# Kernel optimization log

Hardware: AMD Instinct MI355X
Metric: run time of the kernel (lower is better)

## Reference

```python
import jax, jax.numpy as jnp
import numpy as np

IN_DIM = 256
HID = 384
HEADS = 6
NH1 = HID // HEADS  # 64 per-head hidden in layer1
N = 3072
SLOPE_GAT = 0.2   # LeakyReLU inside GAT attention
SLOPE_ACT = 0.01  # default nn.LeakyReLU / F.leaky_relu slope


def _leaky(x, s):
    return jnp.where(x >= 0, x, s * x)


def _gat_sublayer(h, mask, W, a, heads, nh, concat):
    # h: [N, F_in], mask: [N, N] bool, W: [heads*nh, F_in], a: [2*nh]
    n = h.shape[0]
    g = (h @ W.T).reshape(n, heads, nh)  # [N, H, F]
    # e[i,j,h] = leakyrelu(<g_i, a_l> + <g_j, a_r>)  (avoids O(N^2) concat)
    sl = jnp.einsum('nhf,f->nh', g, a[:nh])
    sr = jnp.einsum('nhf,f->nh', g, a[nh:])
    e = _leaky(sl[:, None, :] + sr[None, :, :], SLOPE_GAT)  # [N, N, H]
    e = jnp.where(mask[:, :, None], e, jnp.float32(-10000.0))
    att = jax.nn.softmax(e, axis=1)  # softmax over source nodes j
    out = jnp.einsum('ijh,jhf->ihf', att, g)
    return out.reshape(n, heads * nh) if concat else out.mean(axis=1)


def _gat(x, mask, W1, a1, W2, a2):
    x = _gat_sublayer(x, mask, W1, a1, HEADS, NH1, True)   # [N, HID]
    x = jax.nn.elu(x)
    return _gat_sublayer(x, mask, W2, a2, 1, IN_DIM, False)  # [N, IN_DIM]


def setup_inputs() -> dict:
    key = jax.random.key(0)
    ks = iter(jax.random.split(key, 32))
    d = {
        'feature': jax.random.normal(next(ks), (1, N, IN_DIM), jnp.float32),
        'adj': jax.random.randint(next(ks), (1, N, N), 0, 2, jnp.int32),
        'doc_num': 16,
        'sect_num': 192,
    }
    def w(shape, scale=0.05):
        return jax.random.normal(next(ks), shape, jnp.float32) * scale
    for br in ('sent', 'sect', 'doc'):
        d[f'W1_{br}'] = w((HID, IN_DIM))
        d[f'a1_{br}'] = w((2 * NH1,))
        d[f'W2_{br}'] = w((IN_DIM, HID))
        d[f'a2_{br}'] = w((2 * IN_DIM,))
    d['fusion_W'] = w((IN_DIM, 3 * IN_DIM)); d['fusion_b'] = jnp.zeros((IN_DIM,), jnp.float32)
    d['ffn_W0'] = w((HID, IN_DIM)); d['ffn_b0'] = jnp.zeros((HID,), jnp.float32)
    d['ffn_W1'] = w((HID, HID)); d['ffn_b1'] = jnp.zeros((HID,), jnp.float32)
    d['ffn_W2'] = w((IN_DIM, HID)); d['ffn_b2'] = jnp.zeros((IN_DIM,), jnp.float32)
    return d


def reference(feature, adj, doc_num, sect_num,
              W1_sent, a1_sent, W2_sent, a2_sent,
              W1_sect, a1_sect, W2_sect, a2_sect,
              W1_doc, a1_doc, W2_doc, a2_doc,
              fusion_W, fusion_b,
              ffn_W0, ffn_b0, ffn_W1, ffn_b1, ffn_W2, ffn_b2):
    f = feature[0]          # [N, D]
    n = f.shape[0]
    A = adj[0] != 0         # [N, N]
    cols = jnp.arange(n)
    sent_mask = A & (cols < n - sect_num - doc_num)[None, :]
    sect_mask = A & (cols >= n - sect_num - doc_num)[None, :] & (cols < n - doc_num)[None, :]
    doc_mask = A & (cols >= n - doc_num)[None, :]

    f_sent = _gat(f, sent_mask, W1_sent, a1_sent, W2_sent, a2_sent) + f
    f_sect = _gat(f, sect_mask, W1_sect, a1_sect, W2_sect, a2_sect) + f
    f_doc = _gat(f, doc_mask, W1_doc, a1_doc, W2_doc, a2_doc) + f

    fused = jnp.concatenate([f_doc, f_sect, f_sent], axis=-1)  # [N, 3D]
    fused = _leaky(fused @ fusion_W.T + fusion_b, SLOPE_ACT)
    h = _leaky(fused @ ffn_W0.T + ffn_b0, SLOPE_ACT)
    h = _leaky(h @ ffn_W1.T + ffn_b1, SLOPE_ACT)
    h = _leaky(h @ ffn_W2.T + ffn_b2, SLOPE_ACT)
    return (h + f)[None]    # [1, N, D]
```

## Files before the change

### kernel.cpp

```cpp
#include <hip/hip_runtime.h>
#include <stdint.h>

#define N_NODES 3072
#define D_IN    256
#define HIDDEN  384
#define HEADS   6
#define NH1     64
#define C1      1152
#define C2      768
#define MASK_ULL   48
#define MASK_BYTES 384
#define MASK_BSTRIDE ((size_t)N_NODES * MASK_BYTES)
#define CHUNK   1536
#define MAXQ    2
#define LOG2E   1.4426950408889634f

typedef __bf16 bf16;
typedef __bf16 bf16x8 __attribute__((ext_vector_type(8)));
typedef __bf16 bf16x4 __attribute__((ext_vector_type(4)));
typedef float  f32x4  __attribute__((ext_vector_type(4)));

__device__ __forceinline__ void atomAddF(float* p, float v) {
  __hip_atomic_fetch_add(p, v, __ATOMIC_RELAXED, __HIP_MEMORY_SCOPE_AGENT);
}
__device__ __forceinline__ float fexp2(float x) {
  float r; asm("v_exp_f32 %0, %1" : "=v"(r) : "v"(x)); return r;
}

struct CastArgs {
  const float* src[11];
  bf16*        dst[11];
  int          cum4[12];
};

__global__ __launch_bounds__(256) void cast_all_kernel(CastArgs A) {
  int g = blockIdx.x * 256 + threadIdx.x;
  int j = 0;
#pragma unroll
  for (int k = 1; k < 11; ++k) j += (g >= A.cum4[k]);
  int e = (g - A.cum4[j]) * 4;
  float4 v = *(const float4*)(A.src[j] + e);
  bf16x4 o = { (bf16)v.x, (bf16)v.y, (bf16)v.z, (bf16)v.w };
  *(bf16x4*)(A.dst[j] + e) = o;
}

__global__ __launch_bounds__(256) void pack_adj_kernel(const int* __restrict__ adj,
                                                       unsigned long long* __restrict__ maskU,
                                                       const int* __restrict__ dnum,
                                                       const int* __restrict__ snum) {
  int dn = dnum[0], sn = snum[0];
  int bb1 = N_NODES - sn - dn, bb2 = N_NODES - dn;
  int row = blockIdx.x;
  const int* ar = adj + (size_t)row * N_NODES;
  int lane = threadIdx.x & 63, wave = threadIdx.x >> 6;
#pragma unroll
  for (int it = 0; it < N_NODES / 256; ++it) {
    int j = it * 256 + wave * 64 + lane;
    bool a = ar[j] != 0;
    unsigned long long m0 = __ballot(a && (j < bb1));
    unsigned long long m1 = __ballot(a && (j >= bb1) && (j < bb2));
    unsigned long long m2 = __ballot(a && (j >= bb2));
    if (lane == 0) {
      size_t o = (size_t)row * MASK_ULL + it * 4 + wave;
      maskU[o] = m0;
      maskU[o + (size_t)N_NODES * MASK_ULL] = m1;
      maskU[o + 2 * (size_t)N_NODES * MASK_ULL] = m2;
    }
  }
}

template<int C>
__global__ __launch_bounds__(256) void pack_kernel(const bf16* __restrict__ src,
                                                   bf16* __restrict__ dst) {
  __shared__ bf16 t[64][72];
  int j0 = blockIdx.x * 64, f0 = blockIdx.y * 64;
  int rr = threadIdx.x >> 4;
  int cc = (threadIdx.x & 15) * 4;
#pragma unroll
  for (int p = 0; p < 4; ++p) {
    int r = p * 16 + rr;
    *(bf16x4*)&t[r][cc] = *(const bf16x4*)&src[(size_t)(j0 + r) * C + f0 + cc];
  }
  __syncthreads();
  int f = threadIdx.x & 63, g = threadIdx.x >> 6;
#pragma unroll
  for (int q = 0; q < 2; ++q) {
    int p = g * 2 + q;
    bf16x8 v = { t[p*8+0][f], t[p*8+1][f], t[p*8+2][f], t[p*8+3][f],
                 t[p*8+4][f], t[p*8+5][f], t[p*8+6][f], t[p*8+7][f] };
    *(bf16x8*)&dst[ ((size_t)((j0 >> 3) + p) * C + f0 + f) * 8 ] = v;
  }
}

template<int NHEADS, int NH>
__global__ __launch_bounds__(256) void head_proj_kernel(
    const bf16* __restrict__ g, int ldg,
    const float* __restrict__ a0, const float* __restrict__ a1, const float* __restrict__ a2,
    float* __restrict__ sl, float* __restrict__ sr) {
  int tid = blockIdx.x * 256 + threadIdx.x;
  int c = tid / N_NODES, i = tid - c * N_NODES;
  int b = c / NHEADS, h = c - b * NHEADS;
  const float* a = (b == 0) ? a0 : (b == 1) ? a1 : a2;
  const bf16* gr = g + (size_t)i * ldg + b * (NHEADS * NH) + h * NH;
  float accl = 0.f, accr = 0.f;
#pragma unroll 4
  for (int f = 0; f < NH; f += 4) {
    bf16x4 v = *(const bf16x4*)&gr[f];
#pragma unroll
    for (int k = 0; k < 4; ++k) {
      float gv = (float)v[k];
      accl += gv * a[f + k];
      accr += gv * a[NH + f + k];
    }
  }
  sl[c * N_NODES + i] = accl * LOG2E;
  sr[c * N_NODES + i] = accr * LOG2E;
}

__global__ __launch_bounds__(256) void colmean_kernel(const bf16* __restrict__ g, int C,
                                                      float* __restrict__ out) {
  int c = blockIdx.x * 256 + threadIdx.x;
  if (c >= C) return;
  int r0 = blockIdx.y * 128;
  float s = 0.f;
  for (int r = r0; r < r0 + 128; ++r) s += (float)g[(size_t)r * C + c];
  atomAddF(&out[c], s * (1.0f / N_NODES));
}

template<bool BIAS, bool LEAKY, bool RES, bool F32OUT>
__global__ __launch_bounds__(256) void gemm64_kernel(
    const bf16* __restrict__ A, int lda, int aZoff,
    const bf16* __restrict__ B0, const bf16* __restrict__ B1, const bf16* __restrict__ B2,
    int ldb, void* __restrict__ Cout, int ldc, int cZoff, int K,
    const float* __restrict__ bias, const float* __restrict__ res) {
  __shared__ bf16 As[64 * 64];
  __shared__ bf16 Bs[64 * 64];
  int z = blockIdx.z;
  const bf16* Ab = A + (size_t)z * aZoff;
  const bf16* Bb = (z == 0) ? B0 : (z == 1) ? B1 : B2;
  int m0 = blockIdx.x * 64, n0 = blockIdx.y * 64;
  int tid = threadIdx.x;
  int lane = tid & 63, wave = tid >> 6;
  int wm = wave >> 1, wn = wave & 1;
  int l15 = lane & 15, lk = lane >> 4;
  f32x4 acc[2][2] = {};
  for (int kt = 0; kt < K; kt += 64) {
#pragma unroll
    for (int h = 0; h < 2; ++h) {
      int u = h * 256 + tid;
      int r = u >> 3, up = u & 7;
      int ul = up ^ (r & 7);
      *(bf16x8*)&As[r * 64 + up * 8] = *(const bf16x8*)&Ab[(size_t)(m0 + r) * lda + kt + ul * 8];
      *(bf16x8*)&Bs[r * 64 + up * 8] = *(const bf16x8*)&Bb[(size_t)(n0 + r) * ldb + kt + ul * 8];
    }
    __syncthreads();
#pragma unroll
    for (int s = 0; s < 2; ++s) {
      bf16x8 af[2], bfr[2];
      int u = s * 4 + lk;
#pragma unroll
      for (int mi = 0; mi < 2; ++mi) {
        int r = wm * 32 + mi * 16 + l15;
        af[mi] = *(const bf16x8*)&As[r * 64 + (u ^ (r & 7)) * 8];
      }
#pragma unroll
      for (int ni = 0; ni < 2; ++ni) {
        int r = wn * 32 + ni * 16 + l15;
        bfr[ni] = *(const bf16x8*)&Bs[r * 64 + (u ^ (r & 7)) * 8];
      }
#pragma unroll
      for (int mi = 0; mi < 2; ++mi)
#pragma unroll
        for (int ni = 0; ni < 2; ++ni)
          acc[mi][ni] = __builtin_amdgcn_mfma_f32_16x16x32_bf16(af[mi], bfr[ni], acc[mi][ni], 0, 0, 0);
    }
    __syncthreads();
  }
#pragma unroll
  for (int mi = 0; mi < 2; ++mi)
#pragma unroll
    for (int ni = 0; ni < 2; ++ni)
#pragma unroll
      for (int r = 0; r < 4; ++r) {
        int i = m0 + wm * 32 + mi * 16 + lk * 4 + r;
        int col = z * cZoff + n0 + wn * 32 + ni * 16 + l15;
        float v = acc[mi][ni][r];
        if (BIAS) v += bias[col];
        if (LEAKY) v = (v >= 0.f) ? v : 0.01f * v;
        if (RES) v += res[(size_t)i * ldc + col];
        if (F32OUT) ((float*)Cout)[(size_t)i * ldc + col] = v;
        else        ((bf16*)Cout)[(size_t)i * ldc + col] = (bf16)v;
      }
}

template<bool L1>
__global__ __launch_bounds__(256) void att_kernel(
    const bf16* __restrict__ gP, const float* __restrict__ slA, const float* __restrict__ srA,
    const unsigned char* __restrict__ maskB,
    const int* __restrict__ dnum, const int* __restrict__ snum,
    float* __restrict__ accP, float* __restrict__ lP) {
  constexpr int C = L1 ? C1 : C2;
  int c = blockIdx.y;
  int b = L1 ? (c / 6) : (c >> 2);
  int colbase = L1 ? c * 64 : (b * 256 + (c & 3) * 64);
  int sidx = L1 ? c : b;
  int q = blockIdx.z;
  int dn = dnum[0], sn = snum[0];
  int bb1 = N_NODES - sn - dn, bb2 = N_NODES - dn;
  int jlo = (b == 0) ? 0 : (b == 1) ? bb1 : bb2;
  int jhi = (b == 0) ? bb1 : (b == 1) ? bb2 : N_NODES;
  int lo32 = jlo & ~31, hi32 = (jhi + 31) & ~31;
  int qlo = q * CHUNK, qhi = qlo + CHUNK;
  int wlo = max(lo32, qlo), whi = min(hi32, qhi);
  if (wlo >= whi) return;

  int wave = threadIdx.x >> 6, lane = threadIdx.x & 63;
  int l15 = lane & 15, lk = lane >> 4;
  int row0 = blockIdx.x * 64 + wave * 16;
  int ip = row0 + l15;
  float sl = slA[sidx * N_NODES + ip];
  const float* srp = srA + sidx * N_NODES;
  const unsigned char* mrow = maskB + (size_t)b * MASK_BSTRIDE + (size_t)ip * MASK_BYTES;
  bf16x8 ones;
#pragma unroll
  for (int e = 0; e < 8; ++e) ones[e] = (bf16)1.0f;
  f32x4 acc[4] = {};
  f32x4 accl = {};
  for (int jt = wlo; jt < whi; jt += 32) {
    int jb = jt + lk * 8;
    unsigned int mb = mrow[jb >> 3];
    float4 s0 = *(const float4*)&srp[jb];
    float4 s1 = *(const float4*)&srp[jb + 4];
    float sv[8] = { s0.x, s0.y, s0.z, s0.w, s1.x, s1.y, s1.z, s1.w };
    bf16x8 a8;
#pragma unroll
    for (int e = 0; e < 8; ++e) {
      float x = sl + sv[e];
      x = fmaf(fminf(x, 0.f), -0.8f, x);
      float p = fexp2(x);
      p = ((mb >> e) & 1u) ? p : 0.f;
      a8[e] = (bf16)p;
    }
    size_t pbase = (size_t)(jb >> 3) * C * 8;
#pragma unroll
    for (int nf = 0; nf < 4; ++nf) {
      bf16x8 b8 = *(const bf16x8*)&gP[pbase + (size_t)(colbase + nf * 16 + l15) * 8];
      acc[nf] = __builtin_amdgcn_mfma_f32_16x16x32_bf16(a8, b8, acc[nf], 0, 0, 0);
    }
    accl = __builtin_amdgcn_mfma_f32_16x16x32_bf16(a8, ones, accl, 0, 0, 0);
  }
  int slot = c * MAXQ + q;
  float* ap = accP + ((size_t)slot * N_NODES + row0) * 64;
#pragma unroll
  for (int nf = 0; nf < 4; ++nf)
#pragma unroll
    for (int r = 0; r < 4; ++r)
      ap[(lk * 4 + r) * 64 + nf * 16 + l15] = acc[nf][r];
  if (l15 == 0) {
#pragma unroll
    for (int r = 0; r < 4; ++r)
      lP[(size_t)slot * N_NODES + row0 + lk * 4 + r] = accl[r];
  }
}

__global__ __launch_bounds__(256) void fin1_kernel(
    const float* __restrict__ accP, const float* __restrict__ lP,
    const float* __restrict__ gm, const int* __restrict__ dnum, const int* __restrict__ snum,
    bf16* __restrict__ out1) {
  int t = blockIdx.x * 256 + threadIdx.x;
  int i = t / (C1 / 8), f0 = (t - i * (C1 / 8)) * 8;
  int c = f0 >> 6;
  int b = c / 6;
  int dn = dnum[0], sn = snum[0];
  int bb1 = N_NODES - sn - dn, bb2 = N_NODES - dn;
  int jlo = (b == 0) ? 0 : (b == 1) ? bb1 : bb2;
  int jhi = (b == 0) ? bb1 : (b == 1) ? bb2 : N_NODES;
  float l = 0.f;
  float a[8] = {0.f,0.f,0.f,0.f,0.f,0.f,0.f,0.f};
  if (jhi > jlo) {
    int q0 = jlo / CHUNK, q1 = (jhi - 1) / CHUNK;
    for (int q = q0; q <= q1; ++q) {
      int slot = c * MAXQ + q;
      l += lP[(size_t)slot * N_NODES + i];
      const float* ap = &accP[((size_t)slot * N_NODES + i) * 64 + (f0 & 63)];
      f32x4 v0 = *(const f32x4*)ap, v1 = *(const f32x4*)(ap + 4);
#pragma unroll
      for (int e = 0; e < 4; ++e) { a[e] += v0[e]; a[e + 4] += v1[e]; }
    }
  }
  float inv = (l > 0.f) ? 1.f / l : 0.f;
  bf16x8 o;
#pragma unroll
  for (int e = 0; e < 8; ++e) {
    float v = (l > 0.f) ? a[e] * inv : gm[f0 + e];
    v = (v > 0.f) ? v : (__expf(v) - 1.f);
    o[e] = (bf16)v;
  }
  *(bf16x8*)&out1[(size_t)i * C1 + f0] = o;
}

__global__ __launch_bounds__(256) void fin2_kernel(
    const float* __restrict__ accP, const float* __restrict__ lP,
    const float* __restrict__ gm, const float* __restrict__ feat,
    const int* __restrict__ dnum, const int* __restrict__ snum,
    bf16* __restrict__ fused) {
  int t = blockIdx.x * 256 + threadIdx.x;
  int i = t / (C2 / 8), f0 = (t - i * (C2 / 8)) * 8;
  int b = f0 >> 8;
  int fi = f0 & 255;
  int fc = (f0 >> 6) & 3;
  int c = b * 4 + fc;
  int dn = dnum[0], sn = snum[0];
  int bb1 = N_NODES - sn - dn, bb2 = N_NODES - dn;
  int jlo = (b == 0) ? 0 : (b == 1) ? bb1 : bb2;
  int jhi = (b == 0) ? bb1 : (b == 1) ? bb2 : N_NODES;
  float l = 0.f;
  float a[8] = {0.f,0.f,0.f,0.f,0.f,0.f,0.f,0.f};
  if (jhi > jlo) {
    int q0 = jlo / CHUNK, q1 = (jhi - 1) / CHUNK;
    for (int q = q0; q <= q1; ++q) {
      int slot = c * MAXQ + q;
      l += lP[(size_t)slot * N_NODES + i];
      const float* ap = &accP[((size_t)slot * N_NODES + i) * 64 + (f0 & 63)];
      f32x4 v0 = *(const f32x4*)ap, v1 = *(const f32x4*)(ap + 4);
#pragma unroll
      for (int e = 0; e < 4; ++e) { a[e] += v0[e]; a[e + 4] += v1[e]; }
    }
  }
  float inv = (l > 0.f) ? 1.f / l : 0.f;
  bf16x8 o;
#pragma unroll
  for (int e = 0; e < 8; ++e) {
    float v = (l > 0.f) ? a[e] * inv : gm[f0 + e];
    v += feat[(size_t)i * D_IN + fi + e];
    o[e] = (bf16)v;
  }
  *(bf16x8*)&fused[(size_t)i * C2 + (2 - b) * D_IN + fi] = o;
}

extern "C" void kernel_launch(void* const* d_in, const int* in_sizes, int n_in,
                              void* d_out, int out_size, void* d_ws, size_t ws_size,
                              hipStream_t stream) {
  (void)in_sizes; (void)n_in; (void)out_size; (void)ws_size;
  const float* feature = (const float*)d_in[0];
  const int*   adj     = (const int*)d_in[1];
  const int*   dnum    = (const int*)d_in[2];
  const int*   snum    = (const int*)d_in[3];
  const float* W1s = (const float*)d_in[4];  const float* a1s = (const float*)d_in[5];
  const float* W2s = (const float*)d_in[6];  const float* a2s = (const float*)d_in[7];
  const float* W1e = (const float*)d_in[8];  const float* a1e = (const float*)d_in[9];
  const float* W2e = (const float*)d_in[10]; const float* a2e = (const float*)d_in[11];
  const float* W1d = (const float*)d_in[12]; const float* a1d = (const float*)d_in[13];
  const float* W2d = (const float*)d_in[14]; const float* a2d = (const float*)d_in[15];
  const float* fW  = (const float*)d_in[16]; const float* fB  = (const float*)d_in[17];
  const float* w0  = (const float*)d_in[18]; const float* b0  = (const float*)d_in[19];
  const float* w1  = (const float*)d_in[20]; const float* b1  = (const float*)d_in[21];
  const float* w2  = (const float*)d_in[22]; const float* b2  = (const float*)d_in[23];

  char* ws = (char*)d_ws;
  size_t off = 0;
  auto alloc = [&](size_t bytes) { void* p = ws + off; off += (bytes + 255) & ~(size_t)255; return p; };

  unsigned long long* maskU = (unsigned long long*)alloc(3 * (size_t)N_NODES * MASK_ULL * 8);
  bf16* fbf   = (bf16*)alloc((size_t)N_NODES * D_IN * 2);
  bf16* w1b0  = (bf16*)alloc(HIDDEN * D_IN * 2);
  bf16* w1b1  = (bf16*)alloc(HIDDEN * D_IN * 2);
  bf16* w1b2  = (bf16*)alloc(HIDDEN * D_IN * 2);
  bf16* w2b0  = (bf16*)alloc(D_IN * HIDDEN * 2);
  bf16* w2b1  = (bf16*)alloc(D_IN * HIDDEN * 2);
  bf16* w2b2  = (bf16*)alloc(D_IN * HIDDEN * 2);
  bf16* wfusb = (bf16*)alloc(D_IN * C2 * 2);
  bf16* wf0b  = (bf16*)alloc(HIDDEN * D_IN * 2);
  bf16* wf1b  = (bf16*)alloc(HIDDEN * HIDDEN * 2);
  bf16* wf2b  = (bf16*)alloc(D_IN * HIDDEN * 2);
  bf16* g1    = (bf16*)alloc((size_t)N_NODES * C1 * 2);
  bf16* gP1   = (bf16*)alloc((size_t)N_NODES * C1 * 2);
  bf16* out1  = (bf16*)alloc((size_t)N_NODES * C1 * 2);
  bf16* g2    = (bf16*)alloc((size_t)N_NODES * C2 * 2);
  bf16* gP2   = (bf16*)alloc((size_t)N_NODES * C2 * 2);
  bf16* fusedB= (bf16*)alloc((size_t)N_NODES * C2 * 2);
  bf16* h0    = (bf16*)alloc((size_t)N_NODES * D_IN * 2);
  bf16* h1    = (bf16*)alloc((size_t)N_NODES * HIDDEN * 2);
  bf16* h2    = (bf16*)alloc((size_t)N_NODES * HIDDEN * 2);
  float* sl1  = (float*)alloc(18 * N_NODES * 4);
  float* sr1  = (float*)alloc(18 * N_NODES * 4);
  float* sl2  = (float*)alloc(3 * N_NODES * 4);
  float* sr2  = (float*)alloc(3 * N_NODES * 4);
  float* accU = (float*)alloc((size_t)18 * MAXQ * N_NODES * 64 * 4);
  float* lU   = (float*)alloc((size_t)18 * MAXQ * N_NODES * 4);
  size_t zoff = off;
  float* gm1  = (float*)alloc(C1 * 4);
  float* gm2  = (float*)alloc(C2 * 4);
  size_t zbytes = off - zoff;
  const unsigned char* maskBytes = (const unsigned char*)maskU;

  hipMemsetAsync(ws + zoff, 0, zbytes, stream);

  CastArgs ca;
  {
    const float* srcs[11] = { feature, W1s, W1e, W1d, W2s, W2e, W2d, fW, w0, w1, w2 };
    bf16* dsts[11] = { fbf, w1b0, w1b1, w1b2, w2b0, w2b1, w2b2, wfusb, wf0b, wf1b, wf2b };
    int counts[11] = { N_NODES*D_IN, HIDDEN*D_IN, HIDDEN*D_IN, HIDDEN*D_IN,
                       D_IN*HIDDEN, D_IN*HIDDEN, D_IN*HIDDEN, D_IN*C2,
                       HIDDEN*D_IN, HIDDEN*HIDDEN, D_IN*HIDDEN };
    int cum = 0;
    for (int k = 0; k < 11; ++k) { ca.src[k] = srcs[k]; ca.dst[k] = dsts[k]; ca.cum4[k] = cum; cum += counts[k] / 4; }
    ca.cum4[11] = cum;
    cast_all_kernel<<<cum / 256, 256, 0, stream>>>(ca);
  }
  pack_adj_kernel<<<N_NODES, 256, 0, stream>>>(adj, maskU, dnum, snum);
  gemm64_kernel<false,false,false,false><<<dim3(48,6,3), 256, 0, stream>>>(
      fbf, D_IN, 0, w1b0, w1b1, w1b2, D_IN, g1, C1, HIDDEN, D_IN, nullptr, nullptr);
  pack_kernel<C1><<<dim3(48,18), 256, 0, stream>>>(g1, gP1);
  head_proj_kernel<HEADS, NH1><<<18 * N_NODES / 256, 256, 0, stream>>>(g1, C1, a1s, a1e, a1d, sl1, sr1);
  colmean_kernel<<<dim3((C1 + 255) / 256, 24), 256, 0, stream>>>(g1, C1, gm1);
  att_kernel<true><<<dim3(48, 18, MAXQ), 256, 0, stream>>>(gP1, sl1, sr1, maskBytes, dnum, snum, accU, lU);
  fin1_kernel<<<N_NODES * (C1 / 8) / 256, 256, 0, stream>>>(accU, lU, gm1, dnum, snum, out1);
  gemm64_kernel<false,false,false,false><<<dim3(48,4,3), 256, 0, stream>>>(
      out1, C1, HIDDEN, w2b0, w2b1, w2b2, HIDDEN, g2, C2, D_IN, HIDDEN, nullptr, nullptr);
  pack_kernel<C2><<<dim3(48,12), 256, 0, stream>>>(g2, gP2);
  head_proj_kernel<1, D_IN><<<3 * N_NODES / 256, 256, 0, stream>>>(g2, C2, a2s, a2e, a2d, sl2, sr2);
  colmean_kernel<<<dim3((C2 + 255) / 256, 24), 256, 0, stream>>>(g2, C2, gm2);
  att_kernel<false><<<dim3(48, 12, MAXQ), 256, 0, stream>>>(gP2, sl2, sr2, maskBytes, dnum, snum, accU, lU);
  fin2_kernel<<<N_NODES * (C2 / 8) / 256, 256, 0, stream>>>(accU, lU, gm2, feature, dnum, snum, fusedB);
  gemm64_kernel<true,true,false,false><<<dim3(48,4,1), 256, 0, stream>>>(
      fusedB, C2, 0, wfusb, wfusb, wfusb, C2, h0, D_IN, 0, C2, fB, nullptr);
  gemm64_kernel<true,true,false,false><<<dim3(48,6,1), 256, 0, stream>>>(
      h0, D_IN, 0, wf0b, wf0b, wf0b, D_IN, h1, HIDDEN, 0, D_IN, b0, nullptr);
  gemm64_kernel<true,true,false,false><<<dim3(48,6,1), 256, 0, stream>>>(
      h1, HIDDEN, 0, wf1b, wf1b, wf1b, HIDDEN, h2, HIDDEN, 0, HIDDEN, b1, nullptr);
  gemm64_kernel<true,true,true,true><<<dim3(48,4,1), 256, 0, stream>>>(
      h2, HIDDEN, 0, wf2b, wf2b, wf2b, HIDDEN, d_out, D_IN, 0, HIDDEN, b2, feature);
}
```

Measured before the change: 310.9 us.

## Factor attention exponentials per node and rebalance source-range split across branches

Replaces the per-edge exp2 of the LeakyReLU score with products of precomputed per-node exponentials (exp(sl)*exp(sr) or their 0.2-scaled versions), chosen by comparing against 1. The source range is now split into four chunks only for the large sentence branch, while the short section and doc ranges get a single chunk, with new slot indexing in the finalize kernels. Head projection is parallelised with 16 lanes per row and a shuffle reduction. This removes transcendental work from the inner loop at the cost of two extra loads per element, and it risks overflow or precision loss because no max is subtracted.

```diff
diff --git a/kernel.cpp b/kernel.cpp
--- a/kernel.cpp
+++ b/kernel.cpp
@@ -11,8 +11,7 @@
 #define MASK_ULL   48
 #define MASK_BYTES 384
 #define MASK_BSTRIDE ((size_t)N_NODES * MASK_BYTES)
-#define CHUNK   1536
-#define MAXQ    2
+#define QS      4
 #define LOG2E   1.4426950408889634f
 
 typedef __bf16 bf16;
@@ -25,6 +24,9 @@
 }
 __device__ __forceinline__ float fexp2(float x) {
   float r; asm("v_exp_f32 %0, %1" : "=v"(r) : "v"(x)); return r;
+}
+__device__ __forceinline__ int bnd32(int jlo, int jhi, int len, int q, int Qb) {
+  return (q >= Qb) ? ((jhi + 31) & ~31) : ((jlo + (len * q) / Qb) & ~31);
 }
 
 struct CastArgs {
@@ -92,29 +94,41 @@
   }
 }
 
-template<int NHEADS, int NH>
+template<int NCPB, int NH>
 __global__ __launch_bounds__(256) void head_proj_kernel(
     const bf16* __restrict__ g, int ldg,
     const float* __restrict__ a0, const float* __restrict__ a1, const float* __restrict__ a2,
-    float* __restrict__ sl, float* __restrict__ sr) {
-  int tid = blockIdx.x * 256 + threadIdx.x;
-  int c = tid / N_NODES, i = tid - c * N_NODES;
-  int b = c / NHEADS, h = c - b * NHEADS;
+    float* __restrict__ elp, float* __restrict__ eln,
+    float* __restrict__ erp, float* __restrict__ ern) {
+  int c = blockIdx.y;
+  int i = blockIdx.x * 16 + (threadIdx.x >> 4);
+  int b = c / NCPB;
   const float* a = (b == 0) ? a0 : (b == 1) ? a1 : a2;
-  const bf16* gr = g + (size_t)i * ldg + b * (NHEADS * NH) + h * NH;
+  int f0 = (threadIdx.x & 15) * (NH / 16);
+  const bf16* gr = g + (size_t)i * ldg + c * NH + f0;
   float accl = 0.f, accr = 0.f;
-#pragma unroll 4
-  for (int f = 0; f < NH; f += 4) {
-    bf16x4 v = *(const bf16x4*)&gr[f];
-#pragma unroll
-    for (int k = 0; k < 4; ++k) {
-      float gv = (float)v[k];
-      accl += gv * a[f + k];
-      accr += gv * a[NH + f + k];
-    }
-  }
-  sl[c * N_NODES + i] = accl * LOG2E;
-  sr[c * N_NODES + i] = accr * LOG2E;
+#pragma unroll
+  for (int k = 0; k < NH / 16; k += 4) {
+    bf16x4 v = *(const bf16x4*)&gr[k];
+#pragma unroll
+    for (int e = 0; e < 4; ++e) {
+      float gv = (float)v[e];
+      accl += gv * a[f0 + k + e];
+      accr += gv * a[NH + f0 + k + e];
+    }
+  }
+#pragma unroll
+  for (int m = 1; m < 16; m <<= 1) {
+    accl += __shfl_xor(accl, m, 64);
+    accr += __shfl_xor(accr, m, 64);
+  }
+  if ((threadIdx.x & 15) == 0) {
+    int o = c * N_NODES + i;
+    elp[o] = fexp2(accl * LOG2E);
+    eln[o] = fexp2(0.2f * accl * LOG2E);
+    erp[o] = fexp2(accr * LOG2E);
+    ern[o] = fexp2(0.2f * accr * LOG2E);
+  }
 }
 
 __global__ __launch_bounds__(256) void colmean_kernel(const bf16* __restrict__ g, int C,
@@ -195,31 +209,38 @@
 
 template<bool L1>
 __global__ __launch_bounds__(256) void att_kernel(
-    const bf16* __restrict__ gP, const float* __restrict__ slA, const float* __restrict__ srA,
+    const bf16* __restrict__ gP,
+    const float* __restrict__ elpA, const float* __restrict__ elnA,
+    const float* __restrict__ erpA, const float* __restrict__ ernA,
     const unsigned char* __restrict__ maskB,
     const int* __restrict__ dnum, const int* __restrict__ snum,
     float* __restrict__ accP, float* __restrict__ lP) {
   constexpr int C = L1 ? C1 : C2;
+  constexpr int NSENT = L1 ? 6 : 4;
   int c = blockIdx.y;
   int b = L1 ? (c / 6) : (c >> 2);
   int colbase = L1 ? c * 64 : (b * 256 + (c & 3) * 64);
   int sidx = L1 ? c : b;
   int q = blockIdx.z;
+  int Qb = (b == 0) ? QS : 1;
+  if (q >= Qb) return;
   int dn = dnum[0], sn = snum[0];
   int bb1 = N_NODES - sn - dn, bb2 = N_NODES - dn;
   int jlo = (b == 0) ? 0 : (b == 1) ? bb1 : bb2;
   int jhi = (b == 0) ? bb1 : (b == 1) ? bb2 : N_NODES;
-  int lo32 = jlo & ~31, hi32 = (jhi + 31) & ~31;
-  int qlo = q * CHUNK, qhi = qlo + CHUNK;
-  int wlo = max(lo32, qlo), whi = min(hi32, qhi);
+  int len = jhi - jlo;
+  int wlo = bnd32(jlo, jhi, len, q, Qb);
+  int whi = bnd32(jlo, jhi, len, q + 1, Qb);
   if (wlo >= whi) return;
 
   int wave = threadIdx.x >> 6, lane = threadIdx.x & 63;
   int l15 = lane & 15, lk = lane >> 4;
   int row0 = blockIdx.x * 64 + wave * 16;
   int ip = row0 + l15;
-  float sl = slA[sidx * N_NODES + ip];
-  const float* srp = srA + sidx * N_NODES;
+  float elp = elpA[sidx * N_NODES + ip];
+  float eln = elnA[sidx * N_NODES + ip];
+  const float* erpB = erpA + sidx * N_NODES;
+  const float* ernB = ernA + sidx * N_NODES;
   const unsigned char* mrow = maskB + (size_t)b * MASK_BSTRIDE + (size_t)ip * MASK_BYTES;
   bf16x8 ones;
 #pragma unroll
@@ -229,15 +250,18 @@
   for (int jt = wlo; jt < whi; jt += 32) {
     int jb = jt + lk * 8;
     unsigned int mb = mrow[jb >> 3];
-    float4 s0 = *(const float4*)&srp[jb];
-    float4 s1 = *(const float4*)&srp[jb + 4];
-    float sv[8] = { s0.x, s0.y, s0.z, s0.w, s1.x, s1.y, s1.z, s1.w };
+    float4 p0 = *(const float4*)&erpB[jb];
+    float4 p1 = *(const float4*)&erpB[jb + 4];
+    float4 n0 = *(const float4*)&ernB[jb];
+    float4 n1 = *(const float4*)&ernB[jb + 4];
+    float pv[8] = { p0.x, p0.y, p0.z, p0.w, p1.x, p1.y, p1.z, p1.w };
+    float nv[8] = { n0.x, n0.y, n0.z, n0.w, n1.x, n1.y, n1.z, n1.w };
     bf16x8 a8;
 #pragma unroll
     for (int e = 0; e < 8; ++e) {
-      float x = sl + sv[e];
-      x = fmaf(fminf(x, 0.f), -0.8f, x);
-      float p = fexp2(x);
+      float z = elp * pv[e];
+      float w = eln * nv[e];
+      float p = (z >= 1.f) ? z : w;
       p = ((mb >> e) & 1u) ? p : 0.f;
       a8[e] = (bf16)p;
     }
@@ -249,7 +273,7 @@
     }
     accl = __builtin_amdgcn_mfma_f32_16x16x32_bf16(a8, ones, accl, 0, 0, 0);
   }
-  int slot = c * MAXQ + q;
+  int slot = (b == 0) ? (c * QS + q) : (NSENT * QS + (c - NSENT));
   float* ap = accP + ((size_t)slot * N_NODES + row0) * 64;
 #pragma unroll
   for (int nf = 0; nf < 4; ++nf)
@@ -275,12 +299,14 @@
   int bb1 = N_NODES - sn - dn, bb2 = N_NODES - dn;
   int jlo = (b == 0) ? 0 : (b == 1) ? bb1 : bb2;
   int jhi = (b == 0) ? bb1 : (b == 1) ? bb2 : N_NODES;
+  int len = jhi - jlo;
+  int Qb = (b == 0) ? QS : 1;
   float l = 0.f;
   float a[8] = {0.f,0.f,0.f,0.f,0.f,0.f,0.f,0.f};
-  if (jhi > jlo) {
-    int q0 = jlo / CHUNK, q1 = (jhi - 1) / CHUNK;
-    for (int q = q0; q <= q1; ++q) {
-      int slot = c * MAXQ + q;
+  if (len > 0) {
+    for (int q = 0; q < Qb; ++q) {
+      if (bnd32(jlo, jhi, len, q, Qb) >= bnd32(jlo, jhi, len, q + 1, Qb)) continue;
+      int slot = (b == 0) ? (c * QS + q) : (6 * QS + (c - 6));
       l += lP[(size_t)slot * N_NODES + i];
       const float* ap = &accP[((size_t)slot * N_NODES + i) * 64 + (f0 & 63)];
       f32x4 v0 = *(const f32x4*)ap, v1 = *(const f32x4*)(ap + 4);
@@ -314,12 +340,14 @@
   int bb1 = N_NODES - sn - dn, bb2 = N_NODES - dn;
   int jlo = (b == 0) ? 0 : (b == 1) ? bb1 : bb2;
   int jhi = (b == 0) ? bb1 : (b == 1) ? bb2 : N_NODES;
+  int len = jhi - jlo;
+  int Qb = (b == 0) ? QS : 1;
   float l = 0.f;
   float a[8] = {0.f,0.f,0.f,0.f,0.f,0.f,0.f,0.f};
-  if (jhi > jlo) {
-    int q0 = jlo / CHUNK, q1 = (jhi - 1) / CHUNK;
-    for (int q = q0; q <= q1; ++q) {
-      int slot = c * MAXQ + q;
+  if (len > 0) {
+    for (int q = 0; q < Qb; ++q) {
+      if (bnd32(jlo, jhi, len, q, Qb) >= bnd32(jlo, jhi, len, q + 1, Qb)) continue;
+      int slot = (b == 0) ? (c * QS + q) : (4 * QS + (c - 4));
       l += lP[(size_t)slot * N_NODES + i];
       const float* ap = &accP[((size_t)slot * N_NODES + i) * 64 + (f0 & 63)];
       f32x4 v0 = *(const f32x4*)ap, v1 = *(const f32x4*)(ap + 4);
@@ -382,12 +410,16 @@
   bf16* h0    = (bf16*)alloc((size_t)N_NODES * D_IN * 2);
   bf16* h1    = (bf16*)alloc((size_t)N_NODES * HIDDEN * 2);
   bf16* h2    = (bf16*)alloc((size_t)N_NODES * HIDDEN * 2);
-  float* sl1  = (float*)alloc(18 * N_NODES * 4);
-  float* sr1  = (float*)alloc(18 * N_NODES * 4);
-  float* sl2  = (float*)alloc(3 * N_NODES * 4);
-  float* sr2  = (float*)alloc(3 * N_NODES * 4);
-  float* accU = (float*)alloc((size_t)18 * MAXQ * N_NODES * 64 * 4);
-  float* lU   = (float*)alloc((size_t)18 * MAXQ * N_NODES * 4);
+  float* elp1 = (float*)alloc(18 * N_NODES * 4);
+  float* eln1 = (float*)alloc(18 * N_NODES * 4);
+  float* erp1 = (float*)alloc(18 * N_NODES * 4);
+  float* ern1 = (float*)alloc(18 * N_NODES * 4);
+  float* elp2 = (float*)alloc(3 * N_NODES * 4);
+  float* eln2 = (float*)alloc(3 * N_NODES * 4);
+  float* erp2 = (float*)alloc(3 * N_NODES * 4);
+  float* ern2 = (float*)alloc(3 * N_NODES * 4);
+  float* accU = (float*)alloc((size_t)36 * N_NODES * 64 * 4);
+  float* lU   = (float*)alloc((size_t)36 * N_NODES * 4);
   size_t zoff = off;
   float* gm1  = (float*)alloc(C1 * 4);
   float* gm2  = (float*)alloc(C2 * 4);
@@ -412,16 +444,16 @@
   gemm64_kernel<false,false,false,false><<<dim3(48,6,3), 256, 0, stream>>>(
       fbf, D_IN, 0, w1b0, w1b1, w1b2, D_IN, g1, C1, HIDDEN, D_IN, nullptr, nullptr);
   pack_kernel<C1><<<dim3(48,18), 256, 0, stream>>>(g1, gP1);
-  head_proj_kernel<HEADS, NH1><<<18 * N_NODES / 256, 256, 0, stream>>>(g1, C1, a1s, a1e, a1d, sl1, sr1);
+  head_proj_kernel<HEADS, NH1><<<dim3(192,18), 256, 0, stream>>>(g1, C1, a1s, a1e, a1d, elp1, eln1, erp1, ern1);
   colmean_kernel<<<dim3((C1 + 255) / 256, 24), 256, 0, stream>>>(g1, C1, gm1);
-  att_kernel<true><<<dim3(48, 18, MAXQ), 256, 0, stream>>>(gP1, sl1, sr1, maskBytes, dnum, snum, accU, lU);
+  att_kernel<true><<<dim3(48, 18, QS), 256, 0, stream>>>(gP1, elp1, eln1, erp1, ern1, maskBytes, dnum, snum, accU, lU);
   fin1_kernel<<<N_NODES * (C1 / 8) / 256, 256, 0, stream>>>(accU, lU, gm1, dnum, snum, out1);
   gemm64_kernel<false,false,false,false><<<dim3(48,4,3), 256, 0, stream>>>(
       out1, C1, HIDDEN, w2b0, w2b1, w2b2, HIDDEN, g2, C2, D_IN, HIDDEN, nullptr, nullptr);
   pack_kernel<C2><<<dim3(48,12), 256, 0, stream>>>(g2, gP2);
-  head_proj_kernel<1, D_IN><<<3 * N_NODES / 256, 256, 0, stream>>>(g2, C2, a2s, a2e, a2d, sl2, sr2);
+  head_proj_kernel<1, D_IN><<<dim3(192,3), 256, 0, stream>>>(g2, C2, a2s, a2e, a2d, elp2, eln2, erp2, ern2);
   colmean_kernel<<<dim3((C2 + 255) / 256, 24), 256, 0, stream>>>(g2, C2, gm2);
-  att_kernel<false><<<dim3(48, 12, MAXQ), 256, 0, stream>>>(gP2, sl2, sr2, maskBytes, dnum, snum, accU, lU);
+  att_kernel<false><<<dim3(48, 12, QS), 256, 0, stream>>>(gP2, elp2, eln2, erp2, ern2, maskBytes, dnum, snum, accU, lU);
   fin2_kernel<<<N_NODES * (C2 / 8) / 256, 256, 0, stream>>>(accU, lU, gm2, feature, dnum, snum, fusedB);
   gemm64_kernel<true,true,false,false><<<dim3(48,4,1), 256, 0, stream>>>(
       fusedB, C2, 0, wfusb, wfusb, wfusb, C2, h0, D_IN, 0, C2, fB, nullptr);
```

Result: slower. 321.0 us (+3.3%).
